# Kernel tuning notes

Hardware: AMD Instinct MI355X
Metric: run time of the kernel (lower is better)

## Reference

```python
import jax, jax.numpy as jnp
import numpy as np

N_INST = 8      # number of instance labels present in target (== len(torch.unique(gt)))
DELTA_V = 0.5
ALPHA = 1.0
CLAMP_MAX = 100000.0


def setup_inputs() -> dict:
    key = jax.random.key(0)
    k1, k2 = jax.random.split(key)
    prediction = jax.random.normal(k1, (4, 16, 512, 512), dtype=jnp.float32)
    target = jax.random.randint(k2, (4, 512, 512), 0, N_INST)  # all labels 0..7 present whp
    return {"prediction": prediction, "target": target}


def _loss(prediction, target):
    B, nf, H, W = prediction.shape
    N = H * W
    pred = prediction.reshape(B, nf, N)                    # [B, nf, N]
    gt = target.reshape(B, N)                              # [B, N]
    # one-hot instance masks (unique sorted labels == arange(N_INST) by construction)
    mask = (gt[:, :, None] == jnp.arange(N_INST)[None, None, :]).astype(pred.dtype)  # [B, N, C]
    counts = mask.sum(axis=1)                              # [B, C] pixels per instance
    # per-instance means: sum of masked embeddings / counts
    means = jnp.einsum('bfn,bnc->bfc', pred, mask) / counts[:, None, :]  # [B, nf, C]
    # mu_expand - pred_masked = mask * (mu - pred); norm over feature dim
    diff = (means[:, :, None, :] - pred[:, :, :, None]) * mask[:, None, :, :]  # [B, nf, N, C]
    sq = jnp.sum(diff * diff, axis=1)                      # [B, N, C]
    # safe sqrt (zero where diff==0, matching torch.norm subgradient)
    d = jnp.where(sq > 0, jnp.sqrt(jnp.where(sq > 0, sq, 1.0)), 0.0)
    dist = jnp.clip(d - DELTA_V, 0.0, CLAMP_MAX) ** 2      # [B, N, C]
    # faithful to source: torch.sum(distance) is a full scalar reduce, then / counts, sum, / C
    l_var = dist.sum(axis=(1, 2)) * (1.0 / counts).sum(axis=1) / N_INST  # [B]
    return ALPHA * jnp.sum(l_var)


def reference(prediction, target):
    return _loss(prediction, target)
```

## Files before the change

### kernel.cpp

```cpp
#include <hip/hip_runtime.h>

#define NF   16
#define C    8
#define NB   4
#define NPIX (512*512)

#define CH      64
#define CPX     (NPIX / CH)
#define SITERS  (CPX / (256 * 4))

#define DG      256
#define DCHUNK  (NPIX / DG)

#define WS_PSUM 0
#define WS_PCNT (NB * NF * CH * 8)
#define WS_POUT (WS_PCNT + NB * CH * 8)

__global__ __launch_bounds__(256) void sums_kernel(const float* __restrict__ pred,
                                                   const int* __restrict__ tgt,
                                                   float* __restrict__ ws) {
    const int t    = threadIdx.x;
    const int lane = t & 63;
    const int wave = t >> 6;
    const int ch   = blockIdx.x;
    const int f    = blockIdx.y;
    const int b    = blockIdx.z;

    const float* pf = pred + ((size_t)b * NF + f) * NPIX + ch * CPX;
    const int*   tg = tgt  + (size_t)b * NPIX + ch * CPX;

    float acc[8];
#pragma unroll
    for (int c = 0; c < 8; ++c) acc[c] = 0.0f;
    float cnt[8];
#pragma unroll
    for (int c = 0; c < 8; ++c) cnt[c] = 0.0f;

#pragma unroll
    for (int it = 0; it < SITERS; ++it) {
        const int px = it * 1024 + t * 4;
        int4   lab = *(const int4*)(tg + px);
        float4 p   = *(const float4*)(pf + px);
        float m0[8], m1[8], m2[8], m3[8];
#pragma unroll
        for (int c = 0; c < 8; ++c) {
            m0[c] = (lab.x == c) ? 1.0f : 0.0f;
            m1[c] = (lab.y == c) ? 1.0f : 0.0f;
            m2[c] = (lab.z == c) ? 1.0f : 0.0f;
            m3[c] = (lab.w == c) ? 1.0f : 0.0f;
        }
#pragma unroll
        for (int c = 0; c < 8; ++c)
            acc[c] += m0[c] * p.x + m1[c] * p.y + m2[c] * p.z + m3[c] * p.w;
        if (f == 0) {
#pragma unroll
            for (int c = 0; c < 8; ++c)
                cnt[c] += m0[c] + m1[c] + m2[c] + m3[c];
        }
    }

#pragma unroll
    for (int off = 32; off > 0; off >>= 1)
#pragma unroll
        for (int c = 0; c < 8; ++c)
            acc[c] += __shfl_xor(acc[c], off);
    if (f == 0) {
#pragma unroll
        for (int off = 32; off > 0; off >>= 1)
#pragma unroll
            for (int c = 0; c < 8; ++c)
                cnt[c] += __shfl_xor(cnt[c], off);
    }

    __shared__ float sred[4][8];
    __shared__ float scred[4][8];
    if (lane == 0) {
#pragma unroll
        for (int c = 0; c < 8; ++c) sred[wave][c] = acc[c];
        if (f == 0)
#pragma unroll
            for (int c = 0; c < 8; ++c) scred[wave][c] = cnt[c];
    }
    __syncthreads();
    if (t < 8)
        ws[WS_PSUM + (((size_t)b * NF + f) * CH + ch) * 8 + t] =
            sred[0][t] + sred[1][t] + sred[2][t] + sred[3][t];
    if (f == 0 && t >= 8 && t < 16) {
        const int c = t - 8;
        ws[WS_PCNT + (b * CH + ch) * 8 + c] =
            scred[0][c] + scred[1][c] + scred[2][c] + scred[3][c];
    }
}

__global__ __launch_bounds__(256) void dist_kernel(const float* __restrict__ pred,
                                                   const int* __restrict__ tgt,
                                                   const float* __restrict__ ws,
                                                   float* __restrict__ pout) {
    __shared__ float sm_p[2][128];
    __shared__ float scnt_p[8][8];
    __shared__ float scnt[8];
    __shared__ float s_means[128];
    __shared__ float s_invs;
    __shared__ float s_red[4];
    const int tid = threadIdx.x;
    const int b   = blockIdx.y;

    if (tid < 64) {
        const int c = tid & 7, grp = tid >> 3;
        float s = 0.0f;
#pragma unroll
        for (int i = 0; i < 8; ++i)
            s += ws[WS_PCNT + (b * CH + grp * 8 + i) * 8 + c];
        scnt_p[grp][c] = s;
    }
    {
        const int fc = tid & 127, half = tid >> 7;
        const int f = fc >> 3, c = fc & 7;
        float s = 0.0f;
#pragma unroll
        for (int i = 0; i < 32; ++i)
            s += ws[WS_PSUM + (((size_t)b * NF + f) * CH + half * 32 + i) * 8 + c];
        sm_p[half][fc] = s;
    }
    __syncthreads();
    if (tid < 8) {
        float s = 0.0f;
#pragma unroll
        for (int grp = 0; grp < 8; ++grp) s += scnt_p[grp][tid];
        scnt[tid] = s;
    }
    __syncthreads();
    if (tid < 128)
        s_means[tid] = (sm_p[0][tid] + sm_p[1][tid]) / scnt[tid & 7];
    if (tid == 0) {
        float iv = 0.0f;
#pragma unroll
        for (int c = 0; c < 8; ++c) iv += 1.0f / scnt[c];
        s_invs = iv;
    }
    __syncthreads();

    const float* predb = pred + (size_t)b * NF * NPIX;
    const int*   tgtb  = tgt  + (size_t)b * NPIX;

    const int base = blockIdx.x * DCHUNK + tid * 4;
    int4 lab = *(const int4*)(tgtb + base);
    float s0 = 0.f, s1 = 0.f, s2 = 0.f, s3 = 0.f;
#pragma unroll
    for (int f = 0; f < NF; ++f) {
        float4 p = *(const float4*)(predb + f * NPIX + base);
        float d0 = s_means[f * C + lab.x] - p.x;
        float d1 = s_means[f * C + lab.y] - p.y;
        float d2 = s_means[f * C + lab.z] - p.z;
        float d3 = s_means[f * C + lab.w] - p.w;
        s0 += d0 * d0; s1 += d1 * d1; s2 += d2 * d2; s3 += d3 * d3;
    }
    float t0 = fminf(fmaxf(sqrtf(s0) - 0.5f, 0.0f), 100000.0f);
    float t1 = fminf(fmaxf(sqrtf(s1) - 0.5f, 0.0f), 100000.0f);
    float t2 = fminf(fmaxf(sqrtf(s2) - 0.5f, 0.0f), 100000.0f);
    float t3 = fminf(fmaxf(sqrtf(s3) - 0.5f, 0.0f), 100000.0f);
    float acc = t0 * t0 + t1 * t1 + t2 * t2 + t3 * t3;

#pragma unroll
    for (int off = 32; off > 0; off >>= 1) acc += __shfl_down(acc, off);
    const int lane = tid & 63, wave = tid >> 6;
    if (lane == 0) s_red[wave] = acc;
    __syncthreads();
    if (tid == 0) {
        float tot = s_red[0] + s_red[1] + s_red[2] + s_red[3];
        pout[b * DG + blockIdx.x] = tot * s_invs * 0.125f;
    }
}

__global__ void final_kernel(const float* __restrict__ pout, float* __restrict__ out) {
    __shared__ float sr[8];
    const int t = threadIdx.x;
    float v = pout[t] + pout[t + 512];
#pragma unroll
    for (int off = 32; off > 0; off >>= 1) v += __shfl_xor(v, off);
    if ((t & 63) == 0) sr[t >> 6] = v;
    __syncthreads();
    if (t == 0) {
        float s = 0.0f;
#pragma unroll
        for (int i = 0; i < 8; ++i) s += sr[i];
        out[0] = s;
    }
}

extern "C" void kernel_launch(void* const* d_in, const int* in_sizes, int n_in,
                              void* d_out, int out_size, void* d_ws, size_t ws_size,
                              hipStream_t stream) {
    const float* pred = (const float*)d_in[0];
    const int*   tgt  = (const int*)d_in[1];
    float* out = (float*)d_out;
    float* ws  = (float*)d_ws;

    sums_kernel<<<dim3(CH, NF, NB), dim3(256), 0, stream>>>(pred, tgt, ws);
    dist_kernel<<<dim3(DG, NB), dim3(256), 0, stream>>>(pred, tgt, ws, ws + WS_POUT);
    final_kernel<<<dim3(1), dim3(512), 0, stream>>>(ws + WS_POUT, out);
}
```

Baseline: 118.7 us.

## Use per-thread LDS atomic bins for class sums and fewer, larger chunks

Replaces the one-hot mask multiply-accumulate over 8 classes in the sums kernel with per-thread shared-memory bins updated by LDS atomicAdd indexed by label. The bins are then combined with a tree reduction in shared memory. The chunk count drops from 64 to 16 per (feature, batch), so each block covers four times as many pixels, and the dist kernel's partial-sum reads are adjusted to match. This cuts ALU work per pixel but adds LDS atomics, a synchronised tree reduction, and fewer blocks (1024), which may lower occupancy and memory-level parallelism in a bandwidth-bound kernel.

```diff
diff --git a/kernel.cpp b/kernel.cpp
--- a/kernel.cpp
+++ b/kernel.cpp
@@ -5,7 +5,7 @@
 #define NB   4
 #define NPIX (512*512)
 
-#define CH      64
+#define CH      16
 #define CPX     (NPIX / CH)
 #define SITERS  (CPX / (256 * 4))
 
@@ -19,6 +19,8 @@
 __global__ __launch_bounds__(256) void sums_kernel(const float* __restrict__ pred,
                                                    const int* __restrict__ tgt,
                                                    float* __restrict__ ws) {
+    __shared__ float s_acc[256 * 8];
+    __shared__ float s_cnt[32];
     const int t    = threadIdx.x;
     const int lane = t & 63;
     const int wave = t >> 6;
@@ -29,66 +31,55 @@
     const float* pf = pred + ((size_t)b * NF + f) * NPIX + ch * CPX;
     const int*   tg = tgt  + (size_t)b * NPIX + ch * CPX;
 
-    float acc[8];
 #pragma unroll
-    for (int c = 0; c < 8; ++c) acc[c] = 0.0f;
+    for (int c = 0; c < 8; ++c) s_acc[t * 8 + c] = 0.0f;
+
     float cnt[8];
 #pragma unroll
     for (int c = 0; c < 8; ++c) cnt[c] = 0.0f;
 
-#pragma unroll
+#pragma unroll 4
     for (int it = 0; it < SITERS; ++it) {
         const int px = it * 1024 + t * 4;
         int4   lab = *(const int4*)(tg + px);
         float4 p   = *(const float4*)(pf + px);
-        float m0[8], m1[8], m2[8], m3[8];
-#pragma unroll
-        for (int c = 0; c < 8; ++c) {
-            m0[c] = (lab.x == c) ? 1.0f : 0.0f;
-            m1[c] = (lab.y == c) ? 1.0f : 0.0f;
-            m2[c] = (lab.z == c) ? 1.0f : 0.0f;
-            m3[c] = (lab.w == c) ? 1.0f : 0.0f;
-        }
-#pragma unroll
-        for (int c = 0; c < 8; ++c)
-            acc[c] += m0[c] * p.x + m1[c] * p.y + m2[c] * p.z + m3[c] * p.w;
+        atomicAdd(&s_acc[t * 8 + lab.x], p.x);
+        atomicAdd(&s_acc[t * 8 + lab.y], p.y);
+        atomicAdd(&s_acc[t * 8 + lab.z], p.z);
+        atomicAdd(&s_acc[t * 8 + lab.w], p.w);
         if (f == 0) {
 #pragma unroll
             for (int c = 0; c < 8; ++c)
-                cnt[c] += m0[c] + m1[c] + m2[c] + m3[c];
+                cnt[c] += ((lab.x == c) ? 1.0f : 0.0f) + ((lab.y == c) ? 1.0f : 0.0f)
+                        + ((lab.z == c) ? 1.0f : 0.0f) + ((lab.w == c) ? 1.0f : 0.0f);
         }
     }
+    __syncthreads();
 
+    for (int s = 128; s > 0; s >>= 1) {
+        if (t < s) {
 #pragma unroll
-    for (int off = 32; off > 0; off >>= 1)
-#pragma unroll
-        for (int c = 0; c < 8; ++c)
-            acc[c] += __shfl_xor(acc[c], off);
+            for (int c = 0; c < 8; ++c)
+                s_acc[t * 8 + c] += s_acc[(t + s) * 8 + c];
+        }
+        __syncthreads();
+    }
+    if (t < 8)
+        ws[WS_PSUM + (((size_t)b * NF + f) * CH + ch) * 8 + t] = s_acc[t];
+
     if (f == 0) {
 #pragma unroll
         for (int off = 32; off > 0; off >>= 1)
 #pragma unroll
             for (int c = 0; c < 8; ++c)
                 cnt[c] += __shfl_xor(cnt[c], off);
-    }
-
-    __shared__ float sred[4][8];
-    __shared__ float scred[4][8];
-    if (lane == 0) {
+        if (lane == 0)
 #pragma unroll
-        for (int c = 0; c < 8; ++c) sred[wave][c] = acc[c];
-        if (f == 0)
-#pragma unroll
-            for (int c = 0; c < 8; ++c) scred[wave][c] = cnt[c];
-    }
-    __syncthreads();
-    if (t < 8)
-        ws[WS_PSUM + (((size_t)b * NF + f) * CH + ch) * 8 + t] =
-            sred[0][t] + sred[1][t] + sred[2][t] + sred[3][t];
-    if (f == 0 && t >= 8 && t < 16) {
-        const int c = t - 8;
-        ws[WS_PCNT + (b * CH + ch) * 8 + c] =
-            scred[0][c] + scred[1][c] + scred[2][c] + scred[3][c];
+            for (int c = 0; c < 8; ++c) s_cnt[wave * 8 + c] = cnt[c];
+        __syncthreads();
+        if (t < 8)
+            ws[WS_PCNT + (b * CH + ch) * 8 + t] =
+                s_cnt[t] + s_cnt[8 + t] + s_cnt[16 + t] + s_cnt[24 + t];
     }
 }
 
@@ -109,8 +100,8 @@
         const int c = tid & 7, grp = tid >> 3;
         float s = 0.0f;
 #pragma unroll
-        for (int i = 0; i < 8; ++i)
-            s += ws[WS_PCNT + (b * CH + grp * 8 + i) * 8 + c];
+        for (int i = 0; i < 2; ++i)
+            s += ws[WS_PCNT + (b * CH + grp * 2 + i) * 8 + c];
         scnt_p[grp][c] = s;
     }
     {
@@ -118,8 +109,8 @@
         const int f = fc >> 3, c = fc & 7;
         float s = 0.0f;
 #pragma unroll
-        for (int i = 0; i < 32; ++i)
-            s += ws[WS_PSUM + (((size_t)b * NF + f) * CH + half * 32 + i) * 8 + c];
+        for (int i = 0; i < 8; ++i)
+            s += ws[WS_PSUM + (((size_t)b * NF + f) * CH + half * 8 + i) * 8 + c];
         sm_p[half][fc] = s;
     }
     __syncthreads();
```

New measurement: 181.7 us. 1.53x slower.

## Cut sums grid to fewer chunks with prefetched loop and front-load dist loads

Applied to the files above, without the earlier changes.

The sums kernel now uses 8 chunks per feature plane instead of 64, so each block runs a longer loop over 8 pixels per thread, with the next iteration's loads issued before the current data is accumulated (software pipelining). The dist kernel's partial-sum reduction shrinks to match, and all 16 feature loads are issued up front before any arithmetic to raise memory-level parallelism. The trade is far fewer blocks in the sums kernel (512 in total), which may hurt occupancy and latency hiding on a GPU with many CUs, plus more registers per thread in the dist kernel.

```diff
diff --git a/kernel.cpp b/kernel.cpp
--- a/kernel.cpp
+++ b/kernel.cpp
@@ -5,9 +5,10 @@
 #define NB   4
 #define NPIX (512*512)
 
-#define CH      64
+#define CH      8
 #define CPX     (NPIX / CH)
-#define SITERS  (CPX / (256 * 4))
+#define PXI     2048
+#define NIT     (CPX / PXI)
 
 #define DG      256
 #define DCHUNK  (NPIX / DG)
@@ -15,6 +16,19 @@
 #define WS_PSUM 0
 #define WS_PCNT (NB * NF * CH * 8)
 #define WS_POUT (WS_PCNT + NB * CH * 8)
+
+__device__ __forceinline__ void acc4(const int4 lab, const float4 p, float acc[8]) {
+#pragma unroll
+    for (int c = 0; c < 8; ++c)
+        acc[c] += ((lab.x == c) ? p.x : 0.0f) + ((lab.y == c) ? p.y : 0.0f)
+                + ((lab.z == c) ? p.z : 0.0f) + ((lab.w == c) ? p.w : 0.0f);
+}
+__device__ __forceinline__ void cnt4(const int4 lab, float cnt[8]) {
+#pragma unroll
+    for (int c = 0; c < 8; ++c)
+        cnt[c] += ((lab.x == c) ? 1.0f : 0.0f) + ((lab.y == c) ? 1.0f : 0.0f)
+                + ((lab.z == c) ? 1.0f : 0.0f) + ((lab.w == c) ? 1.0f : 0.0f);
+}
 
 __global__ __launch_bounds__(256) void sums_kernel(const float* __restrict__ pred,
                                                    const int* __restrict__ tgt,
@@ -29,35 +43,29 @@
     const float* pf = pred + ((size_t)b * NF + f) * NPIX + ch * CPX;
     const int*   tg = tgt  + (size_t)b * NPIX + ch * CPX;
 
-    float acc[8];
-#pragma unroll
-    for (int c = 0; c < 8; ++c) acc[c] = 0.0f;
-    float cnt[8];
-#pragma unroll
-    for (int c = 0; c < 8; ++c) cnt[c] = 0.0f;
-
-#pragma unroll
-    for (int it = 0; it < SITERS; ++it) {
-        const int px = it * 1024 + t * 4;
-        int4   lab = *(const int4*)(tg + px);
-        float4 p   = *(const float4*)(pf + px);
-        float m0[8], m1[8], m2[8], m3[8];
-#pragma unroll
-        for (int c = 0; c < 8; ++c) {
-            m0[c] = (lab.x == c) ? 1.0f : 0.0f;
-            m1[c] = (lab.y == c) ? 1.0f : 0.0f;
-            m2[c] = (lab.z == c) ? 1.0f : 0.0f;
-            m3[c] = (lab.w == c) ? 1.0f : 0.0f;
-        }
-#pragma unroll
-        for (int c = 0; c < 8; ++c)
-            acc[c] += m0[c] * p.x + m1[c] * p.y + m2[c] * p.z + m3[c] * p.w;
-        if (f == 0) {
-#pragma unroll
-            for (int c = 0; c < 8; ++c)
-                cnt[c] += m0[c] + m1[c] + m2[c] + m3[c];
-        }
-    }
+    float acc[8], cnt[8];
+#pragma unroll
+    for (int c = 0; c < 8; ++c) { acc[c] = 0.0f; cnt[c] = 0.0f; }
+
+    const int o = t * 8;
+    int4   lA = *(const int4*)(tg + o);
+    float4 vA = *(const float4*)(pf + o);
+    int4   lB = *(const int4*)(tg + o + 4);
+    float4 vB = *(const float4*)(pf + o + 4);
+
+#pragma unroll 1
+    for (int it = 0; it < NIT - 1; ++it) {
+        const int n = (it + 1) * PXI + o;
+        int4   lA1 = *(const int4*)(tg + n);
+        float4 vA1 = *(const float4*)(pf + n);
+        int4   lB1 = *(const int4*)(tg + n + 4);
+        float4 vB1 = *(const float4*)(pf + n + 4);
+        acc4(lA, vA, acc); acc4(lB, vB, acc);
+        if (f == 0) { cnt4(lA, cnt); cnt4(lB, cnt); }
+        lA = lA1; vA = vA1; lB = lB1; vB = vB1;
+    }
+    acc4(lA, vA, acc); acc4(lB, vB, acc);
+    if (f == 0) { cnt4(lA, cnt); cnt4(lB, cnt); }
 
 #pragma unroll
     for (int off = 32; off > 0; off >>= 1)
@@ -107,19 +115,15 @@
 
     if (tid < 64) {
         const int c = tid & 7, grp = tid >> 3;
-        float s = 0.0f;
-#pragma unroll
-        for (int i = 0; i < 8; ++i)
-            s += ws[WS_PCNT + (b * CH + grp * 8 + i) * 8 + c];
-        scnt_p[grp][c] = s;
+        scnt_p[grp][c] = ws[WS_PCNT + (b * CH + grp) * 8 + c];
     }
     {
         const int fc = tid & 127, half = tid >> 7;
         const int f = fc >> 3, c = fc & 7;
         float s = 0.0f;
 #pragma unroll
-        for (int i = 0; i < 32; ++i)
-            s += ws[WS_PSUM + (((size_t)b * NF + f) * CH + half * 32 + i) * 8 + c];
+        for (int i = 0; i < 4; ++i)
+            s += ws[WS_PSUM + (((size_t)b * NF + f) * CH + half * 4 + i) * 8 + c];
         sm_p[half][fc] = s;
     }
     __syncthreads();
@@ -145,16 +149,20 @@
 
     const int base = blockIdx.x * DCHUNK + tid * 4;
     int4 lab = *(const int4*)(tgtb + base);
+#define LP(i) float4 p##i = *(const float4*)(predb + (i) * NPIX + base);
+    LP(0) LP(1) LP(2) LP(3) LP(4) LP(5) LP(6) LP(7)
+    LP(8) LP(9) LP(10) LP(11) LP(12) LP(13) LP(14) LP(15)
+#undef LP
     float s0 = 0.f, s1 = 0.f, s2 = 0.f, s3 = 0.f;
-#pragma unroll
-    for (int f = 0; f < NF; ++f) {
-        float4 p = *(const float4*)(predb + f * NPIX + base);
-        float d0 = s_means[f * C + lab.x] - p.x;
-        float d1 = s_means[f * C + lab.y] - p.y;
-        float d2 = s_means[f * C + lab.z] - p.z;
-        float d3 = s_means[f * C + lab.w] - p.w;
-        s0 += d0 * d0; s1 += d1 * d1; s2 += d2 * d2; s3 += d3 * d3;
-    }
+#define AC(i) { \
+    float d0 = s_means[(i) * C + lab.x] - p##i.x; \
+    float d1 = s_means[(i) * C + lab.y] - p##i.y; \
+    float d2 = s_means[(i) * C + lab.z] - p##i.z; \
+    float d3 = s_means[(i) * C + lab.w] - p##i.w; \
+    s0 += d0 * d0; s1 += d1 * d1; s2 += d2 * d2; s3 += d3 * d3; }
+    AC(0) AC(1) AC(2) AC(3) AC(4) AC(5) AC(6) AC(7)
+    AC(8) AC(9) AC(10) AC(11) AC(12) AC(13) AC(14) AC(15)
+#undef AC
     float t0 = fminf(fmaxf(sqrtf(s0) - 0.5f, 0.0f), 100000.0f);
     float t1 = fminf(fmaxf(sqrtf(s1) - 0.5f, 0.0f), 100000.0f);
     float t2 = fminf(fmaxf(sqrtf(s2) - 0.5f, 0.0f), 100000.0f);
```

Measured after the change: 119.9 us. About the same (+1.0%).

## Fuse final reduction into dist kernel via last-block atomic counter; fewer sum chunks

Applied to the files above, without the earlier changes.

Removes the separate final reduction kernel: each dist block writes its partial with an atomic, bumps a global counter, and the last block to finish sums all partials and writes the output. This cuts one kernel launch. It also reduces the pixel chunks per (batch, feature) in the sums kernel from 64 to 16 and drops the unroll pragma, so there are fewer, longer-running blocks and less partial data to reduce later. The risk is lower parallelism in the sums kernel (1024 blocks instead of 4096) and reliance on the counter reset in the first kernel.

```diff
diff --git a/kernel.cpp b/kernel.cpp
--- a/kernel.cpp
+++ b/kernel.cpp
@@ -5,16 +5,18 @@
 #define NB   4
 #define NPIX (512*512)
 
-#define CH      64
+#define CH      16
 #define CPX     (NPIX / CH)
 #define SITERS  (CPX / (256 * 4))
 
 #define DG      256
 #define DCHUNK  (NPIX / DG)
+#define NDIST   (DG * NB)
 
 #define WS_PSUM 0
 #define WS_PCNT (NB * NF * CH * 8)
 #define WS_POUT (WS_PCNT + NB * CH * 8)
+#define WS_CNT  (WS_POUT + NDIST)
 
 __global__ __launch_bounds__(256) void sums_kernel(const float* __restrict__ pred,
                                                    const int* __restrict__ tgt,
@@ -26,6 +28,9 @@
     const int f    = blockIdx.y;
     const int b    = blockIdx.z;
 
+    if (ch == 0 && f == 0 && b == 0 && t == 0)
+        ((int*)(ws + WS_CNT))[0] = 0;
+
     const float* pf = pred + ((size_t)b * NF + f) * NPIX + ch * CPX;
     const int*   tg = tgt  + (size_t)b * NPIX + ch * CPX;
 
@@ -36,7 +41,6 @@
 #pragma unroll
     for (int c = 0; c < 8; ++c) cnt[c] = 0.0f;
 
-#pragma unroll
     for (int it = 0; it < SITERS; ++it) {
         const int px = it * 1024 + t * 4;
         int4   lab = *(const int4*)(tg + px);
@@ -94,23 +98,26 @@
 
 __global__ __launch_bounds__(256) void dist_kernel(const float* __restrict__ pred,
                                                    const int* __restrict__ tgt,
-                                                   const float* __restrict__ ws,
-                                                   float* __restrict__ pout) {
+                                                   const float* __restrict__ wsr,
+                                                   float* __restrict__ ws,
+                                                   float* __restrict__ out) {
     __shared__ float sm_p[2][128];
     __shared__ float scnt_p[8][8];
     __shared__ float scnt[8];
     __shared__ float s_means[128];
     __shared__ float s_invs;
     __shared__ float s_red[4];
+    __shared__ int   s_last;
     const int tid = threadIdx.x;
     const int b   = blockIdx.y;
+    const int g   = b * DG + blockIdx.x;
 
     if (tid < 64) {
         const int c = tid & 7, grp = tid >> 3;
         float s = 0.0f;
 #pragma unroll
-        for (int i = 0; i < 8; ++i)
-            s += ws[WS_PCNT + (b * CH + grp * 8 + i) * 8 + c];
+        for (int i = 0; i < 2; ++i)
+            s += wsr[WS_PCNT + (b * CH + grp * 2 + i) * 8 + c];
         scnt_p[grp][c] = s;
     }
     {
@@ -118,8 +125,8 @@
         const int f = fc >> 3, c = fc & 7;
         float s = 0.0f;
 #pragma unroll
-        for (int i = 0; i < 32; ++i)
-            s += ws[WS_PSUM + (((size_t)b * NF + f) * CH + half * 32 + i) * 8 + c];
+        for (int i = 0; i < 8; ++i)
+            s += wsr[WS_PSUM + (((size_t)b * NF + f) * CH + half * 8 + i) * 8 + c];
         sm_p[half][fc] = s;
     }
     __syncthreads();
@@ -167,24 +174,25 @@
     if (lane == 0) s_red[wave] = acc;
     __syncthreads();
     if (tid == 0) {
-        float tot = s_red[0] + s_red[1] + s_red[2] + s_red[3];
-        pout[b * DG + blockIdx.x] = tot * s_invs * 0.125f;
-    }
-}
-
-__global__ void final_kernel(const float* __restrict__ pout, float* __restrict__ out) {
-    __shared__ float sr[8];
-    const int t = threadIdx.x;
-    float v = pout[t] + pout[t + 512];
-#pragma unroll
-    for (int off = 32; off > 0; off >>= 1) v += __shfl_xor(v, off);
-    if ((t & 63) == 0) sr[t >> 6] = v;
-    __syncthreads();
-    if (t == 0) {
-        float s = 0.0f;
-#pragma unroll
-        for (int i = 0; i < 8; ++i) s += sr[i];
-        out[0] = s;
+        float tot = (s_red[0] + s_red[1] + s_red[2] + s_red[3]) * s_invs * 0.125f;
+        atomicExch(&ws[WS_POUT + g], tot);
+        __threadfence();
+        int old = atomicAdd((int*)(ws + WS_CNT), 1);
+        s_last = (old == NDIST - 1) ? 1 : 0;
+    }
+    __syncthreads();
+
+    if (s_last) {
+        float v = 0.0f;
+#pragma unroll
+        for (int i = 0; i < NDIST / 256; ++i)
+            v += atomicAdd(&ws[WS_POUT + i * 256 + tid], 0.0f);
+#pragma unroll
+        for (int off = 32; off > 0; off >>= 1) v += __shfl_xor(v, off);
+        if (lane == 0) s_red[wave] = v;
+        __syncthreads();
+        if (tid == 0)
+            out[0] = s_red[0] + s_red[1] + s_red[2] + s_red[3];
     }
 }
 
@@ -197,6 +205,5 @@
     float* ws  = (float*)d_ws;
 
     sums_kernel<<<dim3(CH, NF, NB), dim3(256), 0, stream>>>(pred, tgt, ws);
-    dist_kernel<<<dim3(DG, NB), dim3(256), 0, stream>>>(pred, tgt, ws, ws + WS_POUT);
-    final_kernel<<<dim3(1), dim3(512), 0, stream>>>(ws + WS_POUT, out);
+    dist_kernel<<<dim3(DG, NB), dim3(256), 0, stream>>>(pred, tgt, ws, ws, out);
 }
```

Result: slower. 145.2 us (+22.4%).
